# Kernel tuning notes

Measured on AMD Instinct MI355X. Metric: run time of the kernel, lower is better.

## Reference

```python
import jax, jax.numpy as jnp
import numpy as np

N_ETYPES = 4


def setup_inputs() -> dict:
    key = jax.random.key(0)
    ks = jax.random.split(key, 6)
    N, E, F = 50000, 800000, 128
    x = jax.random.normal(ks[0], (N, F), dtype=jnp.float32)
    edge_index = jax.random.randint(ks[1], (2, E), 0, N, dtype=jnp.int64)
    edge_type = jax.random.randint(ks[2], (E,), 0, N_ETYPES, dtype=jnp.int64)
    scale = 1.0 / np.sqrt(F)
    W_self = jax.random.normal(ks[3], (N_ETYPES, F, F), dtype=jnp.float32) * scale
    W_neigh = jax.random.normal(ks[4], (N_ETYPES, F, F), dtype=jnp.float32) * scale
    b = jnp.zeros((N_ETYPES, F), dtype=jnp.float32)
    return {"x": x, "edge_index": edge_index, "edge_type": edge_type,
            "W_self": W_self, "W_neigh": W_neigh, "b": b}


def reference(x, edge_index, edge_type, W_self, W_neigh, b):
    # HeteroConv: per-edge-type SageConv (mean aggregation), then mean over types.
    N = x.shape[0]
    src, dst = edge_index[0], edge_index[1]
    msg = x[src]                                   # [E, F] gathered source features
    outs = []
    for t in range(N_ETYPES):                      # small fixed loop over edge types
        w = (edge_type == t).astype(x.dtype)[:, None]          # [E, 1] type mask
        agg = jax.ops.segment_sum(msg * w, dst, num_segments=N)  # [N, F]
        cnt = jax.ops.segment_sum(w, dst, num_segments=N)        # [N, 1]
        mean_agg = agg / jnp.maximum(cnt, 1.0)
        outs.append(x @ W_self[t] + mean_agg @ W_neigh[t] + b[t])
    out = jnp.stack(outs, axis=0)                  # [n_etypes, N, F]
    return out.mean(axis=0)                        # reduction='mean' over edge types
```

## Files before the change

### kernel.cpp

```cpp
#include <hip/hip_runtime.h>

#define FDIM 128
#define NT 4
#define KDIM (FDIM * (NT + 1))
#define GBM 64

#define RSH 6
#define RNODES 64
#define RCAP 1280
#define NBKT 256
#define CHUNK 4096

typedef __attribute__((ext_vector_type(8))) _Float16 h8v;
typedef __attribute__((ext_vector_type(4))) float f4v;

__device__ __forceinline__ unsigned short f2h(float f) {
    _Float16 h = (_Float16)f;
    return __builtin_bit_cast(unsigned short, h);
}
__device__ __forceinline__ void gload_lds16(const void* g, void* l) {
    __builtin_amdgcn_global_load_lds(
        (const __attribute__((address_space(1))) unsigned int*)g,
        (__attribute__((address_space(3))) unsigned int*)l, 16, 0, 0);
}

__global__ __launch_bounds__(256) void x2h(const float* __restrict__ x,
                                           unsigned short* __restrict__ xh, int n4) {
    int i = blockIdx.x * blockDim.x + threadIdx.x;
    if (i < n4) {
        float4 v = reinterpret_cast<const float4*>(x)[i];
        ushort4 o;
        o.x = f2h(v.x);
        o.y = f2h(v.y);
        o.z = f2h(v.z);
        o.w = f2h(v.w);
        reinterpret_cast<ushort4*>(xh)[i] = o;
    }
}

__global__ void mix_weights(const float* __restrict__ Wself,
                            const float* __restrict__ Wneigh,
                            const float* __restrict__ b,
                            unsigned short* __restrict__ WmixT,
                            float* __restrict__ bmean) {
    int i = blockIdx.x * blockDim.x + threadIdx.x;
    if (i >= KDIM * FDIM) return;
    int k = i / FDIM, j = i % FDIM;
    float v;
    if (k < FDIM) {
        v = 0.25f * (Wself[(size_t)(0 * FDIM + k) * FDIM + j] +
                     Wself[(size_t)(1 * FDIM + k) * FDIM + j] +
                     Wself[(size_t)(2 * FDIM + k) * FDIM + j] +
                     Wself[(size_t)(3 * FDIM + k) * FDIM + j]);
    } else {
        int t = (k - FDIM) >> 7;
        int kk = (k - FDIM) & (FDIM - 1);
        v = 0.25f * Wneigh[((size_t)t * FDIM + kk) * FDIM + j];
    }
    WmixT[(size_t)j * KDIM + k] = f2h(v);
    if (i < FDIM) {
        bmean[i] = 0.25f * (b[i] + b[FDIM + i] + b[2 * FDIM + i] + b[3 * FDIM + i]);
    }
}

__global__ __launch_bounds__(256) void k_bin(
    const int* __restrict__ ei, const int* __restrict__ et,
    int* __restrict__ cur, unsigned int* __restrict__ bin,
    int N, int E, int NR) {
    __shared__ int lcnt[1024];
    __shared__ int lpos[1024];
    const int tid = threadIdx.x;
    const int e0 = blockIdx.x * CHUNK;

    for (int b = tid; b < NR; b += 256) lcnt[b] = 0;
    __syncthreads();

    int rs[16];
    unsigned int recs[16];
#pragma unroll
    for (int i = 0; i < 16; ++i) {
        int e = e0 + i * 256 + tid;
        if (e < E) {
            int src = ei[e];
            int dst = ei[E + e];
            int t = et[e];
            rs[i] = dst >> RSH;
            recs[i] = (unsigned int)src |
                      ((unsigned int)(dst & (RNODES - 1)) << 16) |
                      ((unsigned int)t << 22);
            atomicAdd(&lcnt[rs[i]], 1);
        } else {
            rs[i] = -1;
            recs[i] = 0;
        }
    }
    __syncthreads();

    for (int b = tid; b < NR; b += 256) {
        int c = lcnt[b];
        lpos[b] = (c > 0) ? atomicAdd(&cur[b * 16], c) : 0;
    }
    __syncthreads();

#pragma unroll
    for (int i = 0; i < 16; ++i) {
        if (rs[i] >= 0) {
            int p = atomicAdd(&lpos[rs[i]], 1);
            if (p < RCAP) bin[(size_t)rs[i] * RCAP + p] = recs[i];
        }
    }
}

__global__ __launch_bounds__(256) void k_fused(
    const unsigned short* __restrict__ xh, const int* __restrict__ cur,
    const unsigned int* __restrict__ bin, const unsigned short* __restrict__ WmixT,
    const float* __restrict__ bmean, float* __restrict__ out, int N) {
    __shared__ unsigned int recs[RCAP];
    __shared__ unsigned short srcs[RCAP];
    __shared__ int cnts[NBKT];
    __shared__ int scanb[NBKT];
    __shared__ int boff[NBKT];
    __shared__ int cur2[NBKT];
    __shared__ unsigned short magg[RNODES * FDIM];
    __shared__ unsigned short As[GBM * 32];
    __shared__ unsigned short Bs[FDIM * 32];

    const int r = blockIdx.x;
    const int tid = threadIdx.x;

    int K = cur[r * 16];
    if (K > RCAP) K = RCAP;
    for (int i = tid; i < K; i += 256) recs[i] = bin[(size_t)r * RCAP + i];
    cnts[tid] = 0;
    __syncthreads();
    for (int i = tid; i < K; i += 256) {
        unsigned int rec = recs[i];
        int b = ((rec >> 22) << 6) | ((rec >> 16) & 63);
        atomicAdd(&cnts[b], 1);
    }
    __syncthreads();
    int v = cnts[tid];
    scanb[tid] = v;
    __syncthreads();
    for (int off = 1; off < NBKT; off <<= 1) {
        int tv = (tid >= off) ? scanb[tid - off] : 0;
        __syncthreads();
        scanb[tid] += tv;
        __syncthreads();
    }
    boff[tid] = scanb[tid] - v;
    cur2[tid] = scanb[tid] - v;
    __syncthreads();
    for (int i = tid; i < K; i += 256) {
        unsigned int rec = recs[i];
        int b = ((rec >> 22) << 6) | ((rec >> 16) & 63);
        int p = atomicAdd(&cur2[b], 1);
        srcs[p] = (unsigned short)(rec & 0xffffu);
    }

    const int wid = tid >> 6, lane = tid & 63;
    const int wr = wid >> 1, wc = wid & 1;
    const int n0 = r * GBM;
    const int r16 = lane & 15, kg = lane >> 4;
    const int g = tid >> 4, ln = tid & 15;

    f4v acc[2][4];
#pragma unroll
    for (int m = 0; m < 2; ++m)
#pragma unroll
        for (int n = 0; n < 4; ++n) acc[m][n] = (f4v){0.f, 0.f, 0.f, 0.f};
    __syncthreads();

#pragma unroll 1
    for (int ks = 0; ks < 4; ++ks) {
        int k0 = ks * 32;
        {
            int row = tid >> 2, c = tid & 3;
            int cs = c ^ ((row >> 1) & 3);
            int rg = n0 + row; if (rg >= N) rg = N - 1;
            gload_lds16(xh + (size_t)rg * FDIM + k0 + cs * 8, &As[wid * 512]);
        }
#pragma unroll
        for (int p = 0; p < 2; ++p) {
            int ck = p * 256 + tid;
            int col = ck >> 2, c = ck & 3;
            int cs = c ^ ((col >> 1) & 3);
            gload_lds16(WmixT + (size_t)col * KDIM + k0 + cs * 8,
                        &Bs[(p * 4 + wid) * 512]);
        }
        __syncthreads();
        h8v af[2], bfr[4];
#pragma unroll
        for (int m = 0; m < 2; ++m) {
            int row = wr * 32 + m * 16 + r16;
            af[m] = *reinterpret_cast<const h8v*>(
                &As[row * 32 + ((kg ^ ((row >> 1) & 3)) << 3)]);
        }
#pragma unroll
        for (int n = 0; n < 4; ++n) {
            int col = wc * 64 + n * 16 + r16;
            bfr[n] = *reinterpret_cast<const h8v*>(
                &Bs[col * 32 + ((kg ^ ((col >> 1) & 3)) << 3)]);
        }
#pragma unroll
        for (int m = 0; m < 2; ++m)
#pragma unroll
            for (int n = 0; n < 4; ++n)
                acc[m][n] = __builtin_amdgcn_mfma_f32_16x16x32_f16(
                    af[m], bfr[n], acc[m][n], 0, 0, 0);
        __syncthreads();
    }

#pragma unroll 1
    for (int t = 0; t < 4; ++t) {
#pragma unroll 1
        for (int it = 0; it < 4; ++it) {
            int dl = it * 16 + g;
            int b = (t << 6) | dl;
            int beg = boff[b], m = cnts[b];
            h8v a = (h8v)(_Float16)0.f;
            h8v bb = (h8v)(_Float16)0.f;
            int i = 0;
            for (; i + 2 <= m; i += 2) {
                int s0 = srcs[beg + i];
                int s1 = srcs[beg + i + 1];
                a  += *reinterpret_cast<const h8v*>(xh + (size_t)s0 * FDIM + ln * 8);
                bb += *reinterpret_cast<const h8v*>(xh + (size_t)s1 * FDIM + ln * 8);
            }
            if (i < m) {
                int s0 = srcs[beg + i];
                a += *reinterpret_cast<const h8v*>(xh + (size_t)s0 * FDIM + ln * 8);
            }
            float rc = (m > 0) ? 1.0f / (float)m : 0.0f;
            h8v o = (a + bb) * (_Float16)rc;
            *reinterpret_cast<h8v*>(&magg[dl * FDIM + ((ln ^ (dl & 15)) << 3)]) = o;
        }
        __syncthreads();

#pragma unroll 1
        for (int ks = 0; ks < 4; ++ks) {
            int k0 = FDIM + t * FDIM + ks * 32;
#pragma unroll
            for (int p = 0; p < 2; ++p) {
                int ck = p * 256 + tid;
                int col = ck >> 2, c = ck & 3;
                int cs = c ^ ((col >> 1) & 3);
                gload_lds16(WmixT + (size_t)col * KDIM + k0 + cs * 8,
                            &Bs[(p * 4 + wid) * 512]);
            }
            __syncthreads();
            h8v af[2], bfr[4];
#pragma unroll
            for (int m = 0; m < 2; ++m) {
                int row = wr * 32 + m * 16 + r16;
                af[m] = *reinterpret_cast<const h8v*>(
                    &magg[row * FDIM + (((ks * 4 + kg) ^ (row & 15)) << 3)]);
            }
#pragma unroll
            for (int n = 0; n < 4; ++n) {
                int col = wc * 64 + n * 16 + r16;
                bfr[n] = *reinterpret_cast<const h8v*>(
                    &Bs[col * 32 + ((kg ^ ((col >> 1) & 3)) << 3)]);
            }
#pragma unroll
            for (int m = 0; m < 2; ++m)
#pragma unroll
                for (int n = 0; n < 4; ++n)
                    acc[m][n] = __builtin_amdgcn_mfma_f32_16x16x32_f16(
                        af[m], bfr[n], acc[m][n], 0, 0, 0);
            __syncthreads();
        }
    }

    float bm[4];
#pragma unroll
    for (int n = 0; n < 4; ++n) bm[n] = bmean[wc * 64 + n * 16 + r16];
#pragma unroll
    for (int m = 0; m < 2; ++m) {
#pragma unroll
        for (int j = 0; j < 4; ++j) {
            int row = n0 + wr * 32 + m * 16 + kg * 4 + j;
            if (row < N) {
                float* o = out + (size_t)row * FDIM;
#pragma unroll
                for (int n = 0; n < 4; ++n)
                    o[wc * 64 + n * 16 + r16] = acc[m][n][j] + bm[n];
            }
        }
    }
}

extern "C" void kernel_launch(void* const* d_in, const int* in_sizes, int n_in,
                              void* d_out, int out_size, void* d_ws, size_t ws_size,
                              hipStream_t stream) {
    const float* x      = (const float*)d_in[0];
    const int*   ei     = (const int*)d_in[1];
    const int*   et     = (const int*)d_in[2];
    const float* Wself  = (const float*)d_in[3];
    const float* Wneigh = (const float*)d_in[4];
    const float* b      = (const float*)d_in[5];
    float* out = (float*)d_out;

    const int N = in_sizes[0] / FDIM;
    const int E = in_sizes[2];
    const int NR = (N + RNODES - 1) >> RSH;

    char* ws = (char*)d_ws;
    unsigned short* xh    = (unsigned short*)ws;
    unsigned short* WmixT = xh + (size_t)N * FDIM;
    float* bmean = (float*)(WmixT + (size_t)FDIM * KDIM);
    int* cur     = (int*)(bmean + FDIM);
    unsigned int* bin = (unsigned int*)(cur + (size_t)NR * 16);

    hipMemsetAsync(cur, 0, (size_t)NR * 16 * sizeof(int), stream);

    x2h<<<(N * FDIM / 4 + 255) / 256, 256, 0, stream>>>(x, xh, N * FDIM / 4);

    mix_weights<<<(KDIM * FDIM + 255) / 256, 256, 0, stream>>>(Wself, Wneigh, b, WmixT, bmean);

    k_bin<<<(E + CHUNK - 1) / CHUNK, 256, 0, stream>>>(ei, et, cur, bin, N, E, NR);

    k_fused<<<NR, 256, 0, stream>>>(xh, cur, bin, WmixT, bmean, out, N);
}
```

Before: 91.03 us.

## Halve node tile to 32 rows and alias shared memory regions

Shrinks each fused block's tile from 64 to 32 destination nodes. The bin capacity, bucket count, record bit layout, MFMA tiling (one 16-row fragment per wave) and epilogue change to match. Shared buffers are packed into one aliased byte array so LDS use per block drops, and the neighbour gather loop is unrolled by four with an out-of-range node guard. The goal is more blocks and higher occupancy so gather latency is hidden better, at the cost of loading the weight tiles twice as often in total.

```diff
diff --git a/kernel.cpp b/kernel.cpp
--- a/kernel.cpp
+++ b/kernel.cpp
@@ -3,12 +3,12 @@
 #define FDIM 128
 #define NT 4
 #define KDIM (FDIM * (NT + 1))
-#define GBM 64
-
-#define RSH 6
-#define RNODES 64
-#define RCAP 1280
-#define NBKT 256
+#define GBM 32
+
+#define RSH 5
+#define RNODES 32
+#define RCAP 768
+#define NBKT 128
 #define CHUNK 4096
 
 typedef __attribute__((ext_vector_type(8))) _Float16 h8v;
@@ -67,8 +67,8 @@
     const int* __restrict__ ei, const int* __restrict__ et,
     int* __restrict__ cur, unsigned int* __restrict__ bin,
     int N, int E, int NR) {
-    __shared__ int lcnt[1024];
-    __shared__ int lpos[1024];
+    __shared__ int lcnt[2048];
+    __shared__ int lpos[2048];
     const int tid = threadIdx.x;
     const int e0 = blockIdx.x * CHUNK;
 
@@ -87,7 +87,7 @@
             rs[i] = dst >> RSH;
             recs[i] = (unsigned int)src |
                       ((unsigned int)(dst & (RNODES - 1)) << 16) |
-                      ((unsigned int)t << 22);
+                      ((unsigned int)t << 21);
             atomicAdd(&lcnt[rs[i]], 1);
         } else {
             rs[i] = -1;
@@ -115,15 +115,16 @@
     const unsigned short* __restrict__ xh, const int* __restrict__ cur,
     const unsigned int* __restrict__ bin, const unsigned short* __restrict__ WmixT,
     const float* __restrict__ bmean, float* __restrict__ out, int N) {
-    __shared__ unsigned int recs[RCAP];
-    __shared__ unsigned short srcs[RCAP];
-    __shared__ int cnts[NBKT];
-    __shared__ int scanb[NBKT];
-    __shared__ int boff[NBKT];
-    __shared__ int cur2[NBKT];
-    __shared__ unsigned short magg[RNODES * FDIM];
-    __shared__ unsigned short As[GBM * 32];
-    __shared__ unsigned short Bs[FDIM * 32];
+    __shared__ __align__(16) char smem[18944];
+    unsigned int* recs   = (unsigned int*)smem;
+    int* scanb           = (int*)(smem + 3072);
+    int* cur2            = (int*)(smem + 3584);
+    unsigned short* As   = (unsigned short*)smem;
+    unsigned short* magg = (unsigned short*)smem;
+    unsigned short* srcs = (unsigned short*)(smem + 8192);
+    int* cnts            = (int*)(smem + 9728);
+    int* boff            = (int*)(smem + 10240);
+    unsigned short* Bs   = (unsigned short*)(smem + 10752);
 
     const int r = blockIdx.x;
     const int tid = threadIdx.x;
@@ -131,29 +132,28 @@
     int K = cur[r * 16];
     if (K > RCAP) K = RCAP;
     for (int i = tid; i < K; i += 256) recs[i] = bin[(size_t)r * RCAP + i];
-    cnts[tid] = 0;
+    if (tid < NBKT) cnts[tid] = 0;
     __syncthreads();
     for (int i = tid; i < K; i += 256) {
         unsigned int rec = recs[i];
-        int b = ((rec >> 22) << 6) | ((rec >> 16) & 63);
+        int b = ((rec >> 21) << 5) | ((rec >> 16) & 31);
         atomicAdd(&cnts[b], 1);
     }
     __syncthreads();
-    int v = cnts[tid];
-    scanb[tid] = v;
+    int v = (tid < NBKT) ? cnts[tid] : 0;
+    if (tid < NBKT) scanb[tid] = v;
     __syncthreads();
     for (int off = 1; off < NBKT; off <<= 1) {
-        int tv = (tid >= off) ? scanb[tid - off] : 0;
-        __syncthreads();
-        scanb[tid] += tv;
-        __syncthreads();
-    }
-    boff[tid] = scanb[tid] - v;
-    cur2[tid] = scanb[tid] - v;
+        int tv = (tid >= off && tid < NBKT) ? scanb[tid - off] : 0;
+        __syncthreads();
+        if (tid < NBKT) scanb[tid] += tv;
+        __syncthreads();
+    }
+    if (tid < NBKT) { boff[tid] = scanb[tid] - v; cur2[tid] = scanb[tid] - v; }
     __syncthreads();
     for (int i = tid; i < K; i += 256) {
         unsigned int rec = recs[i];
-        int b = ((rec >> 22) << 6) | ((rec >> 16) & 63);
+        int b = ((rec >> 21) << 5) | ((rec >> 16) & 31);
         int p = atomicAdd(&cur2[b], 1);
         srcs[p] = (unsigned short)(rec & 0xffffu);
     }
@@ -164,17 +164,15 @@
     const int r16 = lane & 15, kg = lane >> 4;
     const int g = tid >> 4, ln = tid & 15;
 
-    f4v acc[2][4];
-#pragma unroll
-    for (int m = 0; m < 2; ++m)
-#pragma unroll
-        for (int n = 0; n < 4; ++n) acc[m][n] = (f4v){0.f, 0.f, 0.f, 0.f};
+    f4v acc[4];
+#pragma unroll
+    for (int n = 0; n < 4; ++n) acc[n] = (f4v){0.f, 0.f, 0.f, 0.f};
     __syncthreads();
 
 #pragma unroll 1
     for (int ks = 0; ks < 4; ++ks) {
         int k0 = ks * 32;
-        {
+        if (wid < 2) {
             int row = tid >> 2, c = tid & 3;
             int cs = c ^ ((row >> 1) & 3);
             int rg = n0 + row; if (rg >= N) rg = N - 1;
@@ -189,11 +187,10 @@
                         &Bs[(p * 4 + wid) * 512]);
         }
         __syncthreads();
-        h8v af[2], bfr[4];
-#pragma unroll
-        for (int m = 0; m < 2; ++m) {
-            int row = wr * 32 + m * 16 + r16;
-            af[m] = *reinterpret_cast<const h8v*>(
+        h8v af, bfr[4];
+        {
+            int row = wr * 16 + r16;
+            af = *reinterpret_cast<const h8v*>(
                 &As[row * 32 + ((kg ^ ((row >> 1) & 3)) << 3)]);
         }
 #pragma unroll
@@ -203,37 +200,45 @@
                 &Bs[col * 32 + ((kg ^ ((col >> 1) & 3)) << 3)]);
         }
 #pragma unroll
-        for (int m = 0; m < 2; ++m)
-#pragma unroll
-            for (int n = 0; n < 4; ++n)
-                acc[m][n] = __builtin_amdgcn_mfma_f32_16x16x32_f16(
-                    af[m], bfr[n], acc[m][n], 0, 0, 0);
+        for (int n = 0; n < 4; ++n)
+            acc[n] = __builtin_amdgcn_mfma_f32_16x16x32_f16(af, bfr[n], acc[n], 0, 0, 0);
         __syncthreads();
     }
 
 #pragma unroll 1
     for (int t = 0; t < 4; ++t) {
 #pragma unroll 1
-        for (int it = 0; it < 4; ++it) {
+        for (int it = 0; it < 2; ++it) {
             int dl = it * 16 + g;
-            int b = (t << 6) | dl;
-            int beg = boff[b], m = cnts[b];
-            h8v a = (h8v)(_Float16)0.f;
-            h8v bb = (h8v)(_Float16)0.f;
-            int i = 0;
-            for (; i + 2 <= m; i += 2) {
-                int s0 = srcs[beg + i];
-                int s1 = srcs[beg + i + 1];
-                a  += *reinterpret_cast<const h8v*>(xh + (size_t)s0 * FDIM + ln * 8);
-                bb += *reinterpret_cast<const h8v*>(xh + (size_t)s1 * FDIM + ln * 8);
+            int b = (t << 5) | dl;
+            int dst = n0 + dl;
+            if (dst < N) {
+                int beg = boff[b], m = cnts[b];
+                h8v a0 = (h8v)(_Float16)0.f, a1 = (h8v)(_Float16)0.f;
+                h8v a2 = (h8v)(_Float16)0.f, a3 = (h8v)(_Float16)0.f;
+                int i = 0;
+                for (; i + 4 <= m; i += 4) {
+                    int s0 = srcs[beg + i], s1 = srcs[beg + i + 1];
+                    int s2 = srcs[beg + i + 2], s3 = srcs[beg + i + 3];
+                    a0 += *reinterpret_cast<const h8v*>(xh + (size_t)s0 * FDIM + ln * 8);
+                    a1 += *reinterpret_cast<const h8v*>(xh + (size_t)s1 * FDIM + ln * 8);
+                    a2 += *reinterpret_cast<const h8v*>(xh + (size_t)s2 * FDIM + ln * 8);
+                    a3 += *reinterpret_cast<const h8v*>(xh + (size_t)s3 * FDIM + ln * 8);
+                }
+                if (i + 2 <= m) {
+                    int s0 = srcs[beg + i], s1 = srcs[beg + i + 1];
+                    a0 += *reinterpret_cast<const h8v*>(xh + (size_t)s0 * FDIM + ln * 8);
+                    a1 += *reinterpret_cast<const h8v*>(xh + (size_t)s1 * FDIM + ln * 8);
+                    i += 2;
+                }
+                if (i < m) {
+                    int s0 = srcs[beg + i];
+                    a0 += *reinterpret_cast<const h8v*>(xh + (size_t)s0 * FDIM + ln * 8);
+                }
+                float rc = (m > 0) ? 1.0f / (float)m : 0.0f;
+                h8v o = ((a0 + a1) + (a2 + a3)) * (_Float16)rc;
+                *reinterpret_cast<h8v*>(&magg[dl * FDIM + ((ln ^ (dl & 15)) << 3)]) = o;
             }
-            if (i < m) {
-                int s0 = srcs[beg + i];
-                a += *reinterpret_cast<const h8v*>(xh + (size_t)s0 * FDIM + ln * 8);
-            }
-            float rc = (m > 0) ? 1.0f / (float)m : 0.0f;
-            h8v o = (a + bb) * (_Float16)rc;
-            *reinterpret_cast<h8v*>(&magg[dl * FDIM + ((ln ^ (dl & 15)) << 3)]) = o;
         }
         __syncthreads();
 
@@ -249,11 +254,10 @@
                             &Bs[(p * 4 + wid) * 512]);
             }
             __syncthreads();
-            h8v af[2], bfr[4];
-#pragma unroll
-            for (int m = 0; m < 2; ++m) {
-                int row = wr * 32 + m * 16 + r16;
-                af[m] = *reinterpret_cast<const h8v*>(
+            h8v af, bfr[4];
+            {
+                int row = wr * 16 + r16;
+                af = *reinterpret_cast<const h8v*>(
                     &magg[row * FDIM + (((ks * 4 + kg) ^ (row & 15)) << 3)]);
             }
 #pragma unroll
@@ -263,11 +267,8 @@
                     &Bs[col * 32 + ((kg ^ ((col >> 1) & 3)) << 3)]);
             }
 #pragma unroll
-            for (int m = 0; m < 2; ++m)
-#pragma unroll
-                for (int n = 0; n < 4; ++n)
-                    acc[m][n] = __builtin_amdgcn_mfma_f32_16x16x32_f16(
-                        af[m], bfr[n], acc[m][n], 0, 0, 0);
+            for (int n = 0; n < 4; ++n)
+                acc[n] = __builtin_amdgcn_mfma_f32_16x16x32_f16(af, bfr[n], acc[n], 0, 0, 0);
             __syncthreads();
         }
     }
@@ -276,16 +277,13 @@
 #pragma unroll
     for (int n = 0; n < 4; ++n) bm[n] = bmean[wc * 64 + n * 16 + r16];
 #pragma unroll
-    for (int m = 0; m < 2; ++m) {
-#pragma unroll
-        for (int j = 0; j < 4; ++j) {
-            int row = n0 + wr * 32 + m * 16 + kg * 4 + j;
-            if (row < N) {
-                float* o = out + (size_t)row * FDIM;
-#pragma unroll
-                for (int n = 0; n < 4; ++n)
-                    o[wc * 64 + n * 16 + r16] = acc[m][n][j] + bm[n];
-            }
+    for (int j = 0; j < 4; ++j) {
+        int row = n0 + wr * 16 + kg * 4 + j;
+        if (row < N) {
+            float* o = out + (size_t)row * FDIM;
+#pragma unroll
+            for (int n = 0; n < 4; ++n)
+                o[wc * 64 + n * 16 + r16] = acc[n][j] + bm[n];
         }
     }
 }
```

Measured after the change: 96.25 us. 5.7% more time.
